# Performance work log

Measured on AMD Instinct MI355X. Metric: run time of the kernel, lower is better.

Reference implementation:

```python
import jax, jax.numpy as jnp
import numpy as np

N_NODES = 100000
N_EDGES = 1600000
IN_FEAT = 128
HIDDEN = 64
OUT_EMB = 64
N_GRAPHS = 256
PD_EPS = 1e-6  # torch PairwiseDistance eps added to the difference


def gcn_conv(x, src, dst, W, b):
    """PyG GCNConv: h = x@W, add self-loops, sym-normalized scatter-add, + bias."""
    n = x.shape[0]
    h = x @ W  # [N, out]
    loops = jnp.arange(n)
    s = jnp.concatenate([src, loops])
    d = jnp.concatenate([dst, loops])
    deg = jnp.zeros((n,), h.dtype).at[d].add(1.0)
    dinv = jnp.where(deg > 0, jax.lax.rsqrt(jnp.maximum(deg, 1.0)), 0.0)
    norm = (dinv[s] * dinv[d])[:, None]  # [E+N, 1]
    out = jnp.zeros_like(h).at[d].add(norm * h[s])  # gather + scatter-add
    return out + b


def mean_pool(x, batch, num_graphs):
    s = jax.ops.segment_sum(x, batch, num_segments=num_graphs)
    cnt = jax.ops.segment_sum(jnp.ones((x.shape[0],), x.dtype), batch,
                              num_segments=num_graphs)
    return s / jnp.maximum(cnt, 1.0)[:, None]


def tower(x, edge_index, batch, params, num_graphs):
    W1, b1, W2, b2, W3, b3, Wlin, blin = params
    src, dst = edge_index[0], edge_index[1]
    x = jax.nn.relu(gcn_conv(x, src, dst, W1, b1))
    x = jax.nn.relu(gcn_conv(x, src, dst, W2, b2))
    x = gcn_conv(x, src, dst, W3, b3)
    x = mean_pool(x, batch, num_graphs)
    # dropout omitted for determinism (eval mode)
    return x @ Wlin + blin


def setup_inputs() -> dict:
    key = jax.random.key(0)
    ks = jax.random.split(key, 16)

    def glorot(k, fan_in, fan_out):
        lim = np.sqrt(6.0 / (fan_in + fan_out))
        return jax.random.uniform(k, (fan_in, fan_out), jnp.float32, -lim, lim)

    return {
        "x1": jax.random.normal(ks[0], (N_NODES, IN_FEAT), jnp.float32),
        "edge_index1": jax.random.randint(ks[1], (2, N_EDGES), 0, N_NODES),
        "batch1": jnp.sort(jax.random.randint(ks[2], (N_NODES,), 0, N_GRAPHS)),
        "x2": jax.random.normal(ks[3], (N_NODES, IN_FEAT), jnp.float32),
        "edge_index2": jax.random.randint(ks[4], (2, N_EDGES), 0, N_NODES),
        "batch2": jnp.sort(jax.random.randint(ks[5], (N_NODES,), 0, N_GRAPHS)),
        "W1": glorot(ks[6], IN_FEAT, HIDDEN),
        "b1": jnp.zeros((HIDDEN,), jnp.float32),
        "W2": glorot(ks[7], HIDDEN, HIDDEN),
        "b2": jnp.zeros((HIDDEN,), jnp.float32),
        "W3": glorot(ks[8], HIDDEN, HIDDEN),
        "b3": jnp.zeros((HIDDEN,), jnp.float32),
        "Wlin": glorot(ks[9], HIDDEN, OUT_EMB),
        "blin": jnp.zeros((OUT_EMB,), jnp.float32),
        "num_graphs": N_GRAPHS,
    }


def reference(x1, edge_index1, batch1, x2, edge_index2, batch2,
              W1, b1, W2, b2, W3, b3, Wlin, blin, num_graphs):
    params = (W1, b1, W2, b2, W3, b3, Wlin, blin)
    e1 = tower(x1, edge_index1, batch1, params, num_graphs)  # [G, OUT_EMB]
    e2 = tower(x2, edge_index2, batch2, params, num_graphs)
    diff = e1 - e2 + PD_EPS
    return jnp.sqrt(jnp.sum(diff * diff, axis=-1))  # L2 PairwiseDistance, [G]
```

## Files before the change

### kernel.cpp

```cpp
#include <hip/hip_runtime.h>
#include <hip/hip_bf16.h>
#include <math.h>

#define NGRAPHS 256
#define PD_EPS 1e-6f
#define POOL_CHUNK 64
#define NCOLOR 16
#define CSHIFT 4
#define KB 96

typedef __hip_bfloat16 bf16;
typedef unsigned short ushort_t;
typedef short bf8_t __attribute__((ext_vector_type(8)));
typedef float f4_t __attribute__((ext_vector_type(4)));

static __device__ __forceinline__ int wave_uniform(int v) {
  return __builtin_amdgcn_readfirstlane(v);
}
static __device__ __forceinline__ float b2f(bf16 h) { return __bfloat162float(h); }
static __device__ __forceinline__ bf16 f2b(float f) { return __float2bfloat16(f); }
static __device__ __forceinline__ short f2bbits(float f) {
  bf16 h = __float2bfloat16(f);
  return *reinterpret_cast<short*>(&h);
}

__global__ __launch_bounds__(256) void k_count_part(const int* __restrict__ dst1,
                                                    const int* __restrict__ dst2,
                                                    ushort_t* __restrict__ partial1,
                                                    ushort_t* __restrict__ partial2,
                                                    int E, int n, int rng) {
  extern __shared__ int hist[];
  const int tbase = NCOLOR * KB;
  int tower = blockIdx.x >= tbase;
  int bid = blockIdx.x - (tower ? tbase : 0);
  const int* dst = tower ? dst2 : dst1;
  ushort_t* partial = tower ? partial2 : partial1;
  int color = bid & (NCOLOR - 1);
  int sub = bid >> CSHIFT;
  int base = color * rng;
  int hi = n - base; if (hi > rng) hi = rng;
  for (int i = threadIdx.x; i < rng; i += 256) hist[i] = 0;
  __syncthreads();
  const int stride = KB * 256;
  int e = sub * 256 + threadIdx.x;
  for (; e + 7 * stride < E; e += 8 * stride) {
    int d[8];
#pragma unroll
    for (int k = 0; k < 8; ++k) d[k] = dst[e + k * stride] - base;
#pragma unroll
    for (int k = 0; k < 8; ++k)
      if ((unsigned)d[k] < (unsigned)hi) atomicAdd(&hist[d[k]], 1);
  }
  for (; e < E; e += stride) {
    int d = dst[e] - base;
    if ((unsigned)d < (unsigned)hi) atomicAdd(&hist[d], 1);
  }
  __syncthreads();
  ushort_t* outp = partial + (size_t)bid * rng;
  for (int i = threadIdx.x; i < rng; i += 256) outp[i] = (ushort_t)hist[i];
}

__global__ void k_reduce_part(ushort_t* __restrict__ partial1,
                              ushort_t* __restrict__ partial2, int* __restrict__ cnt,
                              float* __restrict__ dinv, int n, int npad, int rng) {
  int gi = blockIdx.x * 256 + threadIdx.x;
  int tower = gi >= npad;
  int li = gi - (tower ? npad : 0);
  if (li >= n) { cnt[gi] = 0; return; }
  ushort_t* partial = tower ? partial2 : partial1;
  int c = li / rng, lli = li - c * rng;
  int acc = 0;
  for (int s = 0; s < KB; ++s) {
    size_t idx = (size_t)(s * NCOLOR + c) * rng + lli;
    int t = partial[idx];
    partial[idx] = (ushort_t)acc;
    acc += t;
  }
  cnt[gi] = acc;
  dinv[tower * n + li] = 1.0f / sqrtf((float)(acc + 1));
}

__global__ void k_scan1(const int* __restrict__ cnt, int* __restrict__ off,
                        int* __restrict__ bsums, int n, int npad) {
  __shared__ int s[256];
  int tid = threadIdx.x;
  int gid = blockIdx.x * 256 + tid;
  int v = cnt[gid];
  s[tid] = v; __syncthreads();
  for (int o = 1; o < 256; o <<= 1) {
    int t = (tid >= o) ? s[tid - o] : 0;
    __syncthreads();
    s[tid] += t;
    __syncthreads();
  }
  int tower = gid >= npad;
  int li = gid - (tower ? npad : 0);
  if (li < n) off[tower * (n + 1) + li] = s[tid] - v;
  if (tid == 255) bsums[blockIdx.x] = s[255];
}

__global__ void k_scan2(int* __restrict__ bsums, int nb, int segstart) {
  __shared__ int s[1024];
  __shared__ int seg0;
  int tid = threadIdx.x;
  int v = (tid < nb) ? bsums[tid] : 0;
  s[tid] = v; __syncthreads();
  for (int o = 1; o < 1024; o <<= 1) {
    int t = (tid >= o) ? s[tid - o] : 0;
    __syncthreads();
    s[tid] += t;
    __syncthreads();
  }
  int excl = s[tid] - v;
  if (tid == segstart) seg0 = excl;
  __syncthreads();
  if (tid < nb) bsums[tid] = (tid >= segstart) ? excl - seg0 : excl;
}

__global__ void k_off_final(int* __restrict__ off, const int* __restrict__ bsums,
                            int n, int npad, int E) {
  int gid = blockIdx.x * 256 + threadIdx.x;
  int tower = gid >= npad;
  int li = gid - (tower ? npad : 0);
  if (li < n) off[tower * (n + 1) + li] += bsums[blockIdx.x];
  if (li == 0) off[tower * (n + 1) + n] = E;
}

__global__ __launch_bounds__(256) void k_fill_col(const int* __restrict__ src1,
                                                  const int* __restrict__ dst1,
                                                  const int* __restrict__ src2,
                                                  const int* __restrict__ dst2,
                                                  const int* __restrict__ off,
                                                  const ushort_t* __restrict__ partial1,
                                                  const ushort_t* __restrict__ partial2,
                                                  int* __restrict__ csr, int E, int n,
                                                  int rng) {
  extern __shared__ int cur[];
  const int tbase = NCOLOR * KB;
  int tower = blockIdx.x >= tbase;
  int bid = blockIdx.x - (tower ? tbase : 0);
  const int* src = tower ? src2 : src1;
  const int* dst = tower ? dst2 : dst1;
  const ushort_t* partial = tower ? partial2 : partial1;
  const int* offt = off + tower * (n + 1);
  int cbase = tower ? E : 0;
  int nodeoff = tower ? n : 0;
  int color = bid & (NCOLOR - 1);
  int sub = bid >> CSHIFT;
  int base = color * rng;
  int hi = n - base; if (hi > rng) hi = rng;
  const ushort_t* pp = partial + (size_t)bid * rng;
  for (int i = threadIdx.x; i < hi; i += 256)
    cur[i] = offt[base + i] + (int)pp[i] + cbase;
  __syncthreads();
  const int stride = KB * 256;
  int e = sub * 256 + threadIdx.x;
  for (; e + 7 * stride < E; e += 8 * stride) {
    int d[8], s[8];
#pragma unroll
    for (int k = 0; k < 8; ++k) d[k] = dst[e + k * stride] - base;
#pragma unroll
    for (int k = 0; k < 8; ++k) s[k] = src[e + k * stride];
#pragma unroll
    for (int k = 0; k < 8; ++k) {
      if ((unsigned)d[k] < (unsigned)hi) {
        int p = atomicAdd(&cur[d[k]], 1);
        csr[p] = s[k] + nodeoff;
      }
    }
  }
  for (; e < E; e += stride) {
    int d = dst[e] - base;
    if ((unsigned)d < (unsigned)hi) {
      int p = atomicAdd(&cur[d], 1);
      csr[p] = src[e] + nodeoff;
    }
  }
}

template <int K, int INF32>
__global__ __launch_bounds__(256, 2) void k_gemm_mfma(const float* __restrict__ xf1,
                                                      const float* __restrict__ xf2,
                                                      const bf16* __restrict__ xb,
                                                      const float* __restrict__ Wg,
                                                      const float* __restrict__ dinv,
                                                      bf16* __restrict__ out, int n2,
                                                      int nper) {
  constexpr int KS = K / 32;
  int lane = threadIdx.x & 63;
  int quad = lane >> 4;
  int col = lane & 15;

  bf8_t bfrag[4][KS];
#pragma unroll
  for (int c = 0; c < 4; ++c)
#pragma unroll
    for (int s = 0; s < KS; ++s)
#pragma unroll
      for (int j = 0; j < 8; ++j)
        bfrag[c][s][j] = f2bbits(Wg[(s * 32 + quad * 8 + j) * 64 + c * 16 + col]);

  int wid = (blockIdx.x * blockDim.x + threadIdx.x) >> 6;
  int nw = (gridDim.x * blockDim.x) >> 6;
  int tiles = (n2 + 15) >> 4;
  for (int t = wid; t < tiles; t += nw) {
    int base = t << 4;
    int arow = base + col;
    if (arow >= n2) arow = n2 - 1;

    bf8_t afrag[KS];
    if (INF32) {
      int tower = arow >= nper;
      const float* xr = (tower ? xf2 : xf1) +
                        (size_t)(arow - (tower ? nper : 0)) * K;
#pragma unroll
      for (int s = 0; s < KS; ++s) {
        float4 u0 = *(const float4*)(xr + s * 32 + quad * 8);
        float4 u1 = *(const float4*)(xr + s * 32 + quad * 8 + 4);
        afrag[s][0] = f2bbits(u0.x);
        afrag[s][1] = f2bbits(u0.y);
        afrag[s][2] = f2bbits(u0.z);
        afrag[s][3] = f2bbits(u0.w);
        afrag[s][4] = f2bbits(u1.x);
        afrag[s][5] = f2bbits(u1.y);
        afrag[s][6] = f2bbits(u1.z);
        afrag[s][7] = f2bbits(u1.w);
      }
    } else {
      const bf16* xr = xb + (size_t)arow * K;
#pragma unroll
      for (int s = 0; s < KS; ++s)
        afrag[s] = *(const bf8_t*)(xr + s * 32 + quad * 8);
    }

    f4_t acc[4];
#pragma unroll
    for (int c = 0; c < 4; ++c) acc[c] = (f4_t){0.f, 0.f, 0.f, 0.f};
#pragma unroll
    for (int s = 0; s < KS; ++s)
#pragma unroll
      for (int c = 0; c < 4; ++c)
        acc[c] = __builtin_amdgcn_mfma_f32_16x16x32_bf16(afrag[s], bfrag[c][s],
                                                         acc[c], 0, 0, 0);
#pragma unroll
    for (int r = 0; r < 4; ++r) {
      int row = base + quad * 4 + r;
      if (row < n2) {
        float sc = dinv[row];
#pragma unroll
        for (int c = 0; c < 4; ++c)
          out[(size_t)row * 64 + c * 16 + col] = f2b(acc[c][r] * sc);
      }
    }
  }
}

template <int MODE>
__global__ __launch_bounds__(256) void k_agg(const bf16* __restrict__ hp,
                                             const int* __restrict__ off,
                                             const int* __restrict__ csr,
                                             const float* __restrict__ dinv,
                                             const float* __restrict__ bias,
                                             void* __restrict__ outv, int n2,
                                             int nper, int E) {
  int lane = threadIdx.x & 63;
  int wid = (blockIdx.x * blockDim.x + threadIdx.x) >> 6;
  int nw = (gridDim.x * blockDim.x) >> 6;
  float b = (MODE == 2) ? 0.f : bias[lane];
  for (int node = wid; node < n2; node += nw) {
    int un = wave_uniform(node);
    int tower = un >= nper;
    int ln = un - (tower ? nper : 0);
    const int* o = off + tower * (nper + 1);
    int cb = tower ? E : 0;
    int beg = o[ln] + cb, end = o[ln + 1] + cb;
    float acc = b2f(hp[(size_t)un * 64 + lane]);
    int e = beg;
    int efull = beg + ((end - beg) & ~7);
    for (; e < efull; e += 8) {
      int s0 = csr[e + 0], s1 = csr[e + 1], s2 = csr[e + 2], s3 = csr[e + 3];
      int s4 = csr[e + 4], s5 = csr[e + 5], s6 = csr[e + 6], s7 = csr[e + 7];
      float a0 = b2f(hp[(size_t)s0 * 64 + lane]);
      float a1 = b2f(hp[(size_t)s1 * 64 + lane]);
      float a2 = b2f(hp[(size_t)s2 * 64 + lane]);
      float a3 = b2f(hp[(size_t)s3 * 64 + lane]);
      float a4 = b2f(hp[(size_t)s4 * 64 + lane]);
      float a5 = b2f(hp[(size_t)s5 * 64 + lane]);
      float a6 = b2f(hp[(size_t)s6 * 64 + lane]);
      float a7 = b2f(hp[(size_t)s7 * 64 + lane]);
      acc += ((a0 + a1) + (a2 + a3)) + ((a4 + a5) + (a6 + a7));
    }
    int rem = end - e;
    if (rem & 4) {
      int s0 = csr[e + 0], s1 = csr[e + 1], s2 = csr[e + 2], s3 = csr[e + 3];
      float a0 = b2f(hp[(size_t)s0 * 64 + lane]);
      float a1 = b2f(hp[(size_t)s1 * 64 + lane]);
      float a2 = b2f(hp[(size_t)s2 * 64 + lane]);
      float a3 = b2f(hp[(size_t)s3 * 64 + lane]);
      acc += (a0 + a1) + (a2 + a3);
      e += 4;
    }
    if (rem & 2) {
      int s0 = csr[e + 0], s1 = csr[e + 1];
      float a0 = b2f(hp[(size_t)s0 * 64 + lane]);
      float a1 = b2f(hp[(size_t)s1 * 64 + lane]);
      acc += a0 + a1;
      e += 2;
    }
    if (rem & 1) {
      acc += b2f(hp[(size_t)csr[e] * 64 + lane]);
    }
    float di = dinv[un];
    if (MODE == 2) {
      ((float*)outv)[(size_t)un * 64 + lane] = acc * di;
    } else {
      float v = fmaf(acc, di, b);
      v = fmaxf(v, 0.f);
      if (MODE == 1) v *= di;
      ((bf16*)outv)[(size_t)un * 64 + lane] = f2b(v);
    }
  }
}

__global__ __launch_bounds__(256) void k_pool(const float* __restrict__ x3,
                                              const int* __restrict__ batch1,
                                              const int* __restrict__ batch2,
                                              float* __restrict__ pooled1,
                                              float* __restrict__ cnt1,
                                              float* __restrict__ pooled2,
                                              float* __restrict__ cnt2, int n,
                                              int wpt) {
  int lane = threadIdx.x & 63;
  int wid = (blockIdx.x * blockDim.x + threadIdx.x) >> 6;
  int tower = wid >= wpt;
  int lw = wid - (tower ? wpt : 0);
  if (lw >= wpt) return;
  int beg = lw * POOL_CHUNK;
  if (beg >= n) return;
  int end = beg + POOL_CHUNK;
  if (end > n) end = n;
  const int* batch = tower ? batch2 : batch1;
  const float* x = x3 + (size_t)(tower ? n : 0) * 64;
  float* pooled = tower ? pooled2 : pooled1;
  float* cnt = tower ? cnt2 : cnt1;

  int cur = wave_uniform(batch[beg]);
  float acc = 0.f;
  int cl = 0;
  int i = beg;
  for (; i + 4 <= end; i += 4) {
    int g0 = wave_uniform(batch[i + 0]);
    int g3 = wave_uniform(batch[i + 3]);
    float a0 = x[(size_t)(i + 0) * 64 + lane];
    float a1 = x[(size_t)(i + 1) * 64 + lane];
    float a2 = x[(size_t)(i + 2) * 64 + lane];
    float a3 = x[(size_t)(i + 3) * 64 + lane];
    if (g0 == cur && g3 == cur) {
      acc += a0 + a1 + a2 + a3;
      cl += 4;
    } else {
      float av[4] = {a0, a1, a2, a3};
#pragma unroll
      for (int k = 0; k < 4; ++k) {
        int g = wave_uniform(batch[i + k]);
        if (g != cur) {
          atomicAdd(&pooled[cur * 64 + lane], acc);
          if (lane == 0) atomicAdd(&cnt[cur], (float)cl);
          acc = 0.f; cl = 0; cur = g;
        }
        acc += av[k];
        cl += 1;
      }
    }
  }
  for (; i < end; ++i) {
    int g = wave_uniform(batch[i]);
    float a = x[(size_t)i * 64 + lane];
    if (g != cur) {
      atomicAdd(&pooled[cur * 64 + lane], acc);
      if (lane == 0) atomicAdd(&cnt[cur], (float)cl);
      acc = 0.f; cl = 0; cur = g;
    }
    acc += a;
    cl += 1;
  }
  atomicAdd(&pooled[cur * 64 + lane], acc);
  if (lane == 0) atomicAdd(&cnt[cur], (float)cl);
}

__global__ void k_final(const float* __restrict__ pooled1, const float* __restrict__ cnt1,
                        const float* __restrict__ pooled2, const float* __restrict__ cnt2,
                        const float* __restrict__ W3, const float* __restrict__ b3,
                        const float* __restrict__ Wlin, const float* __restrict__ blin,
                        float* __restrict__ outp) {
  int g = blockIdx.x;
  int lane = threadIdx.x;
  float c1 = fmaxf(cnt1[g], 1.f), c2 = fmaxf(cnt2[g], 1.f);
  float p1 = pooled1[g * 64 + lane] / c1;
  float p2 = pooled2[g * 64 + lane] / c2;
  float q1 = b3[lane], q2 = b3[lane];
  for (int j = 0; j < 64; ++j) {
    float w = W3[j * 64 + lane];
    q1 = fmaf(__shfl(p1, j), w, q1);
    q2 = fmaf(__shfl(p2, j), w, q2);
  }
  float e1 = blin[lane], e2 = blin[lane];
  for (int j = 0; j < 64; ++j) {
    float w = Wlin[j * 64 + lane];
    e1 = fmaf(__shfl(q1, j), w, e1);
    e2 = fmaf(__shfl(q2, j), w, e2);
  }
  float d = e1 - e2 + PD_EPS;
  float sq = d * d;
  for (int o = 32; o > 0; o >>= 1) sq += __shfl_down(sq, o);
  if (lane == 0) outp[g] = sqrtf(sq);
}

extern "C" void kernel_launch(void* const* d_in, const int* in_sizes, int n_in,
                              void* d_out, int out_size, void* d_ws, size_t ws_size,
                              hipStream_t stream) {
  const float* x1 = (const float*)d_in[0];
  const int* ei1 = (const int*)d_in[1];
  const int* batch1 = (const int*)d_in[2];
  const float* x2 = (const float*)d_in[3];
  const int* ei2 = (const int*)d_in[4];
  const int* batch2 = (const int*)d_in[5];
  const float* W1 = (const float*)d_in[6];
  const float* b1 = (const float*)d_in[7];
  const float* W2 = (const float*)d_in[8];
  const float* b2 = (const float*)d_in[9];
  const float* W3 = (const float*)d_in[10];
  const float* b3 = (const float*)d_in[11];
  const float* Wlin = (const float*)d_in[12];
  const float* blin = (const float*)d_in[13];

  const int N = in_sizes[2];
  const int E = in_sizes[1] / 2;
  const int rng = (N + NCOLOR - 1) / NCOLOR;
  const int nbN = (N + 255) / 256;
  const int Npad = nbN * 256;
  const int nb2 = 2 * nbN;

  const int* src1 = ei1; const int* dst1 = ei1 + E;
  const int* src2 = ei2; const int* dst2 = ei2 + E;

  char* p = (char*)d_ws;
  auto alloc = [&](size_t bytes) {
    char* r = p;
    p += (bytes + 255) & ~(size_t)255;
    return r;
  };
  int* off = (int*)alloc((size_t)2 * (N + 1) * 4);
  int* cntn = (int*)alloc((size_t)2 * Npad * 4);
  int* bsums = (int*)alloc(1024 * 4);
  float* dinv = (float*)alloc((size_t)2 * N * 4);
  int* csr = (int*)alloc((size_t)2 * E * 4);
  ushort_t* partial1 = (ushort_t*)alloc((size_t)NCOLOR * KB * rng * 2);
  ushort_t* partial2 = (ushort_t*)alloc((size_t)NCOLOR * KB * rng * 2);
  bf16* hpA = (bf16*)alloc((size_t)2 * N * 64 * 2);
  bf16* hpB = (bf16*)alloc((size_t)2 * N * 64 * 2);
  float* bufF = (float*)alloc((size_t)2 * N * 64 * 4);
  float* pooled1 = (float*)alloc((size_t)NGRAPHS * 64 * 4);
  float* cnt1 = (float*)alloc((size_t)NGRAPHS * 4);
  float* pooled2 = (float*)alloc((size_t)NGRAPHS * 64 * 4);
  float* cnt2 = (float*)alloc((size_t)NGRAPHS * 4);
  size_t poolspan = (size_t)((char*)(cnt2 + NGRAPHS) - (char*)pooled1);

  const size_t ldsB = (size_t)rng * 4;
  const int N2 = 2 * N;

  hipMemsetAsync(pooled1, 0, poolspan, stream);

  k_count_part<<<2 * NCOLOR * KB, 256, ldsB, stream>>>(dst1, dst2, partial1,
                                                       partial2, E, N, rng);
  k_reduce_part<<<nb2, 256, 0, stream>>>(partial1, partial2, cntn, dinv, N, Npad,
                                         rng);
  k_scan1<<<nb2, 256, 0, stream>>>(cntn, off, bsums, N, Npad);
  k_scan2<<<1, 1024, 0, stream>>>(bsums, nb2, nbN);
  k_off_final<<<nb2, 256, 0, stream>>>(off, bsums, N, Npad, E);
  k_fill_col<<<2 * NCOLOR * KB, 256, ldsB, stream>>>(src1, dst1, src2, dst2, off,
                                                     partial1, partial2, csr, E, N,
                                                     rng);

  k_gemm_mfma<128, 1><<<1024, 256, 0, stream>>>(x1, x2, (const bf16*)nullptr, W1,
                                                dinv, hpA, N2, N);
  k_agg<0><<<4096, 256, 0, stream>>>(hpA, off, csr, dinv, b1, hpB, N2, N, E);
  k_gemm_mfma<64, 0><<<1024, 256, 0, stream>>>((const float*)nullptr,
                                               (const float*)nullptr, hpB, W2, dinv,
                                               hpA, N2, N);
  k_agg<1><<<4096, 256, 0, stream>>>(hpA, off, csr, dinv, b2, hpB, N2, N, E);
  k_agg<2><<<4096, 256, 0, stream>>>(hpB, off, csr, dinv, b3, bufF, N2, N, E);

  const int wpt = (N + POOL_CHUNK - 1) / POOL_CHUNK;
  const int poolBlocks = (2 * wpt + 3) / 4;
  k_pool<<<poolBlocks, 256, 0, stream>>>(bufF, batch1, batch2, pooled1, cnt1,
                                         pooled2, cnt2, N, wpt);

  k_final<<<NGRAPHS, 64, 0, stream>>>(pooled1, cnt1, pooled2, cnt2, W3, b3, Wlin,
                                      blin, (float*)d_out);
}
```

Baseline: 533.7 us.

## Fuse layer-2 GEMM into layer-1 aggregation epilogue via wave shuffles

The separate layer-2 MFMA GEMM launch is removed. Its 64x64 matmul now runs in the epilogue of the layer-1 aggregation kernel: each lane keeps one column of W2 in registers and broadcasts the activated row with shuffles. This saves a kernel launch and a full write and re-read of the intermediate bf16 activations. In exchange it holds 64 extra registers per lane, which can lower occupancy in the latency-bound gather loop, and it replaces matrix-core work with 64 shuffle-FMA steps per node.

```diff
diff --git a/kernel.cpp b/kernel.cpp
--- a/kernel.cpp
+++ b/kernel.cpp
@@ -178,10 +178,9 @@
   }
 }
 
-template <int K, int INF32>
+template <int K>
 __global__ __launch_bounds__(256, 2) void k_gemm_mfma(const float* __restrict__ xf1,
                                                       const float* __restrict__ xf2,
-                                                      const bf16* __restrict__ xb,
                                                       const float* __restrict__ Wg,
                                                       const float* __restrict__ dinv,
                                                       bf16* __restrict__ out, int n2,
@@ -208,29 +207,21 @@
     int arow = base + col;
     if (arow >= n2) arow = n2 - 1;
 
+    int tower = arow >= nper;
+    const float* xr = (tower ? xf2 : xf1) + (size_t)(arow - (tower ? nper : 0)) * K;
     bf8_t afrag[KS];
-    if (INF32) {
-      int tower = arow >= nper;
-      const float* xr = (tower ? xf2 : xf1) +
-                        (size_t)(arow - (tower ? nper : 0)) * K;
-#pragma unroll
-      for (int s = 0; s < KS; ++s) {
-        float4 u0 = *(const float4*)(xr + s * 32 + quad * 8);
-        float4 u1 = *(const float4*)(xr + s * 32 + quad * 8 + 4);
-        afrag[s][0] = f2bbits(u0.x);
-        afrag[s][1] = f2bbits(u0.y);
-        afrag[s][2] = f2bbits(u0.z);
-        afrag[s][3] = f2bbits(u0.w);
-        afrag[s][4] = f2bbits(u1.x);
-        afrag[s][5] = f2bbits(u1.y);
-        afrag[s][6] = f2bbits(u1.z);
-        afrag[s][7] = f2bbits(u1.w);
-      }
-    } else {
-      const bf16* xr = xb + (size_t)arow * K;
-#pragma unroll
-      for (int s = 0; s < KS; ++s)
-        afrag[s] = *(const bf8_t*)(xr + s * 32 + quad * 8);
+#pragma unroll
+    for (int s = 0; s < KS; ++s) {
+      float4 u0 = *(const float4*)(xr + s * 32 + quad * 8);
+      float4 u1 = *(const float4*)(xr + s * 32 + quad * 8 + 4);
+      afrag[s][0] = f2bbits(u0.x);
+      afrag[s][1] = f2bbits(u0.y);
+      afrag[s][2] = f2bbits(u0.z);
+      afrag[s][3] = f2bbits(u0.w);
+      afrag[s][4] = f2bbits(u1.x);
+      afrag[s][5] = f2bbits(u1.y);
+      afrag[s][6] = f2bbits(u1.z);
+      afrag[s][7] = f2bbits(u1.w);
     }
 
     f4_t acc[4];
@@ -252,6 +243,80 @@
           out[(size_t)row * 64 + c * 16 + col] = f2b(acc[c][r] * sc);
       }
     }
+  }
+}
+
+__global__ __launch_bounds__(256) void k_agg_fused(const bf16* __restrict__ hp,
+                                                   const int* __restrict__ off,
+                                                   const int* __restrict__ csr,
+                                                   const float* __restrict__ dinv,
+                                                   const float* __restrict__ bias,
+                                                   const float* __restrict__ W2g,
+                                                   bf16* __restrict__ outv, int n2,
+                                                   int nper, int E) {
+  int lane = threadIdx.x & 63;
+  int wid = (blockIdx.x * blockDim.x + threadIdx.x) >> 6;
+  int nw = (gridDim.x * blockDim.x) >> 6;
+  float b = bias[lane];
+  float w2c[64];
+#pragma unroll
+  for (int k = 0; k < 64; ++k) w2c[k] = W2g[k * 64 + lane];
+
+  for (int node = wid; node < n2; node += nw) {
+    int un = wave_uniform(node);
+    int tower = un >= nper;
+    int ln = un - (tower ? nper : 0);
+    const int* o = off + tower * (nper + 1);
+    int cb = tower ? E : 0;
+    int beg = o[ln] + cb, end = o[ln + 1] + cb;
+    float acc = b2f(hp[(size_t)un * 64 + lane]);
+    int e = beg;
+    int efull = beg + ((end - beg) & ~7);
+    for (; e < efull; e += 8) {
+      int s0 = csr[e + 0], s1 = csr[e + 1], s2 = csr[e + 2], s3 = csr[e + 3];
+      int s4 = csr[e + 4], s5 = csr[e + 5], s6 = csr[e + 6], s7 = csr[e + 7];
+      float a0 = b2f(hp[(size_t)s0 * 64 + lane]);
+      float a1 = b2f(hp[(size_t)s1 * 64 + lane]);
+      float a2 = b2f(hp[(size_t)s2 * 64 + lane]);
+      float a3 = b2f(hp[(size_t)s3 * 64 + lane]);
+      float a4 = b2f(hp[(size_t)s4 * 64 + lane]);
+      float a5 = b2f(hp[(size_t)s5 * 64 + lane]);
+      float a6 = b2f(hp[(size_t)s6 * 64 + lane]);
+      float a7 = b2f(hp[(size_t)s7 * 64 + lane]);
+      acc += ((a0 + a1) + (a2 + a3)) + ((a4 + a5) + (a6 + a7));
+    }
+    int rem = end - e;
+    if (rem & 4) {
+      int s0 = csr[e + 0], s1 = csr[e + 1], s2 = csr[e + 2], s3 = csr[e + 3];
+      float a0 = b2f(hp[(size_t)s0 * 64 + lane]);
+      float a1 = b2f(hp[(size_t)s1 * 64 + lane]);
+      float a2 = b2f(hp[(size_t)s2 * 64 + lane]);
+      float a3 = b2f(hp[(size_t)s3 * 64 + lane]);
+      acc += (a0 + a1) + (a2 + a3);
+      e += 4;
+    }
+    if (rem & 2) {
+      int s0 = csr[e + 0], s1 = csr[e + 1];
+      float a0 = b2f(hp[(size_t)s0 * 64 + lane]);
+      float a1 = b2f(hp[(size_t)s1 * 64 + lane]);
+      acc += a0 + a1;
+      e += 2;
+    }
+    if (rem & 1) {
+      acc += b2f(hp[(size_t)csr[e] * 64 + lane]);
+    }
+    float di = dinv[un];
+    float r1 = fmaxf(fmaf(acc, di, b), 0.f);
+    float h0 = 0.f, h1 = 0.f, h2s = 0.f, h3 = 0.f;
+#pragma unroll
+    for (int k = 0; k < 64; k += 4) {
+      h0 = fmaf(__shfl(r1, k + 0), w2c[k + 0], h0);
+      h1 = fmaf(__shfl(r1, k + 1), w2c[k + 1], h1);
+      h2s = fmaf(__shfl(r1, k + 2), w2c[k + 2], h2s);
+      h3 = fmaf(__shfl(r1, k + 3), w2c[k + 3], h3);
+    }
+    float h = ((h0 + h1) + (h2s + h3)) * di;
+    outv[(size_t)un * 64 + lane] = f2b(h);
   }
 }
 
@@ -316,7 +381,7 @@
     } else {
       float v = fmaf(acc, di, b);
       v = fmaxf(v, 0.f);
-      if (MODE == 1) v *= di;
+      v *= di;
       ((bf16*)outv)[(size_t)un * 64 + lane] = f2b(v);
     }
   }
@@ -482,14 +547,10 @@
                                                      partial1, partial2, csr, E, N,
                                                      rng);
 
-  k_gemm_mfma<128, 1><<<1024, 256, 0, stream>>>(x1, x2, (const bf16*)nullptr, W1,
-                                                dinv, hpA, N2, N);
-  k_agg<0><<<4096, 256, 0, stream>>>(hpA, off, csr, dinv, b1, hpB, N2, N, E);
-  k_gemm_mfma<64, 0><<<1024, 256, 0, stream>>>((const float*)nullptr,
-                                               (const float*)nullptr, hpB, W2, dinv,
-                                               hpA, N2, N);
-  k_agg<1><<<4096, 256, 0, stream>>>(hpA, off, csr, dinv, b2, hpB, N2, N, E);
-  k_agg<2><<<4096, 256, 0, stream>>>(hpB, off, csr, dinv, b3, bufF, N2, N, E);
+  k_gemm_mfma<128><<<1024, 256, 0, stream>>>(x1, x2, W1, dinv, hpA, N2, N);
+  k_agg_fused<<<4096, 256, 0, stream>>>(hpA, off, csr, dinv, b1, W2, hpB, N2, N, E);
+  k_agg<1><<<4096, 256, 0, stream>>>(hpB, off, csr, dinv, b2, hpA, N2, N, E);
+  k_agg<2><<<4096, 256, 0, stream>>>(hpA, off, csr, dinv, b3, bufF, N2, N, E);
 
   const int wpt = (N + POOL_CHUNK - 1) / POOL_CHUNK;
   const int poolBlocks = (2 * wpt + 3) / 4;
```

New measurement: 612.2 us. 14.7% more time.
